# Kernel optimization log

Hardware: AMD Instinct MI355X
Metric: run time of the kernel (lower is better)

The kernel has to match this reference:

```python
import jax, jax.numpy as jnp
import numpy as np

NUM_HEADS = 12


def setup_inputs() -> dict:
    key = jax.random.key(0)
    ks = jax.random.split(key, 6)
    B, N, C = 16, 576, 768
    H, D = NUM_HEADS, 768 // NUM_HEADS
    P = 16
    x = jax.random.normal(ks[0], (B, N, C), dtype=jnp.float32)
    prompt = jax.random.normal(ks[1], (B, 2, P, H, D), dtype=jnp.float32)
    act_scale = jax.random.uniform(ks[2], (2,), dtype=jnp.float32)
    qkv_w = jax.random.normal(ks[3], (3 * C, C), dtype=jnp.float32) * (C ** -0.5)
    proj_w = jax.random.normal(ks[4], (C, C), dtype=jnp.float32) * (C ** -0.5)
    proj_b = jnp.zeros((C,), dtype=jnp.float32)
    return {"x": x, "prompt": prompt, "act_scale": act_scale,
            "qkv_w": qkv_w, "proj_w": proj_w, "proj_b": proj_b}


def reference(x, prompt, act_scale, qkv_w, proj_w, proj_b):
    B, N, C = x.shape
    H = NUM_HEADS
    D = C // H
    scale = D ** -0.5
    # qkv projection: [B,N,3C] -> (3,B,H,N,D)
    qkv = (x @ qkv_w.T).reshape(B, N, 3, H, D).transpose(2, 0, 3, 1, 4)
    q, k, v = qkv[0], qkv[1], qkv[2]
    # prompt: [B,2,P,H,D] -> (2,B,H,P,D)
    pr = jnp.transpose(prompt, (1, 0, 3, 2, 4))
    key_prefix, value_prefix = pr[0], pr[1]        # [B,H,P,D]
    v = jnp.concatenate([value_prefix, v], axis=2)  # [B,H,P+N,D]
    # gated prefix scores
    prompt_attn = jnp.einsum('bhnd,bhpd->bhnp', q, key_prefix) * scale
    prompt_attn = prompt_attn + jnp.tanh(prompt_attn * act_scale[0]) * act_scale[1]
    # standard scores
    attn = jnp.einsum('bhnd,bhmd->bhnm', q, k) * scale
    attn = jnp.concatenate([prompt_attn, attn], axis=-1)  # [B,H,N,P+N]
    attn = jax.nn.softmax(attn, axis=-1)
    out = jnp.einsum('bhnm,bhmd->bhnd', attn, v)  # [B,H,N,D]
    out = out.transpose(0, 2, 1, 3).reshape(B, N, C)
    return out @ proj_w.T + proj_b
```

## Files before the change

### kernel.cpp

```cpp
#include <hip/hip_runtime.h>
#include <hip/hip_bf16.h>
#include <math.h>

namespace {

constexpr int kB = 16, kN = 576, kC = 768, kH = 12, kP = 16;
constexpr int kM = kB * kN;

typedef __attribute__((ext_vector_type(8))) __bf16 bf16x8;
typedef __attribute__((ext_vector_type(4))) float  f32x4;
typedef __attribute__((ext_vector_type(8))) unsigned short u16x8;

__device__ inline unsigned short f2bf(float f) {
  __bf16 h = (__bf16)f;
  return __builtin_bit_cast(unsigned short, h);
}
__device__ inline float bf2f(unsigned short u) {
  unsigned int x = ((unsigned int)u) << 16;
  return __builtin_bit_cast(float, x);
}
__device__ inline unsigned int pk2bf(float lo, float hi) {
  return (unsigned int)f2bf(lo) | ((unsigned int)f2bf(hi) << 16);
}
__device__ inline int xcd_swz(int hw, int nwg) {
  const int per = nwg >> 3;
  return (hw & 7) * per + (hw >> 3);
}

#define GLDS16(src, dst) __builtin_amdgcn_global_load_lds( \
    (const __attribute__((address_space(1))) unsigned int*)(src), \
    (__attribute__((address_space(3))) unsigned int*)(dst), 16, 0, 0)

__global__ __launch_bounds__(256)
void cvt3(const float* __restrict__ x, const float* __restrict__ wq,
          const float* __restrict__ wp, unsigned short* __restrict__ xo,
          unsigned short* __restrict__ wqo, unsigned short* __restrict__ wpo) {
  const int bid = blockIdx.x;
  const float* in; unsigned short* out; int base;
  if (bid < 6912)       { in = x;  out = xo;  base = bid; }
  else if (bid < 8640)  { in = wq; out = wqo; base = bid - 6912; }
  else                  { in = wp; out = wpo; base = bid - 8640; }
  const int i = base * 256 + threadIdx.x;
  const float4 v = ((const float4*)in)[i];
  ((ushort4*)out)[i] = make_ushort4(f2bf(v.x), f2bf(v.y), f2bf(v.z), f2bf(v.w));
}

template<int OB>
__global__ __launch_bounds__(256)
void gemm_bf16(const unsigned short* __restrict__ A, const unsigned short* __restrict__ W,
               const float* __restrict__ bias, void* __restrict__ Yv, int Kd, int Nd) {
  __shared__ __align__(16) unsigned short As[3][4096];
  __shared__ __align__(16) unsigned short Bs[3][4096];
  const int tid  = threadIdx.x;
  const int wv   = tid >> 6, lane = tid & 63;
  const int gx   = Nd >> 7;
  const int lg   = xcd_swz(blockIdx.x, gridDim.x);
  const long bm  = (long)(lg / gx) * 128;
  const long bn  = (long)(lg % gx) * 128;
  const int wr   = (wv >> 1) * 64;
  const int wc   = (wv & 1) * 64;
  const int row15 = lane & 15, kg = lane >> 4;

  auto stage = [&](int buf, int kt) {
#pragma unroll
    for (int site = 0; site < 2; ++site) {
      const int p = site * 256 + tid;
      const unsigned short* srcA = A + (bm + (p >> 2)) * (long)Kd + kt + (p & 3) * 8;
      const unsigned short* srcB = W + (bn + (p >> 2)) * (long)Kd + kt + (p & 3) * 8;
      GLDS16(srcA, &As[buf][site * 2048 + wv * 512]);
      GLDS16(srcB, &Bs[buf][site * 2048 + wv * 512]);
    }
  };

  float bvpre[4] = {0.0f, 0.0f, 0.0f, 0.0f};
  if constexpr (!OB) {
#pragma unroll
    for (int ni = 0; ni < 4; ++ni) bvpre[ni] = bias[bn + wc + ni * 16 + row15];
  }
  asm volatile("s_waitcnt vmcnt(0)" ::: "memory");

  f32x4 acc[4][4] = {};
  stage(0, 0);
  stage(1, 32);

  const int nt = Kd >> 5;
  for (int t = 0; t < nt; ++t) {
    const int cur = t % 3;
    __builtin_amdgcn_sched_barrier(0);
    __builtin_amdgcn_s_barrier();
    if (t + 2 < nt) stage((t + 2) % 3, (t + 2) << 5);
    if (t + 2 < nt)      asm volatile("s_waitcnt vmcnt(8)");
    else if (t + 1 < nt) asm volatile("s_waitcnt vmcnt(4)");
    else                 asm volatile("s_waitcnt vmcnt(0)");
    __builtin_amdgcn_s_barrier();
    __builtin_amdgcn_sched_barrier(0);

    bf16x8 af[4], bf_[4];
#pragma unroll
    for (int mi = 0; mi < 4; ++mi)
      af[mi] = *(const bf16x8*)(&As[cur][(wr + mi * 16 + row15) * 32 + kg * 8]);
#pragma unroll
    for (int ni = 0; ni < 4; ++ni)
      bf_[ni] = *(const bf16x8*)(&Bs[cur][(wc + ni * 16 + row15) * 32 + kg * 8]);
    __builtin_amdgcn_s_setprio(1);
#pragma unroll
    for (int mi = 0; mi < 4; ++mi)
#pragma unroll
      for (int ni = 0; ni < 4; ++ni)
        acc[mi][ni] = __builtin_amdgcn_mfma_f32_16x16x32_bf16(af[mi], bf_[ni], acc[mi][ni], 0, 0, 0);
    __builtin_amdgcn_s_setprio(0);
  }

  const int r4 = kg * 4;
#pragma unroll
  for (int ni = 0; ni < 4; ++ni) {
    const long col = bn + wc + ni * 16 + row15;
    if constexpr (OB) {
      unsigned short* Y = (unsigned short*)Yv;
#pragma unroll
      for (int mi = 0; mi < 4; ++mi)
#pragma unroll
        for (int j = 0; j < 4; ++j)
          Y[(bm + wr + mi * 16 + r4 + j) * (long)Nd + col] = f2bf(acc[mi][ni][j]);
    } else {
      float* Y = (float*)Yv;
#pragma unroll
      for (int mi = 0; mi < 4; ++mi)
#pragma unroll
        for (int j = 0; j < 4; ++j)
          Y[(bm + wr + mi * 16 + r4 + j) * (long)Nd + col] = acc[mi][ni][j] + bvpre[ni];
    }
  }
}

__device__ inline void softmax_group_static(f32x4 (&c)[4], float& lsum,
                                            unsigned short* pl,
                                            const int kg, const int sw) {
  float psum = 0.0f;
#pragma unroll
  for (int kb = 0; kb < 4; ++kb) {
    const float p0 = __expf(c[kb][0] - 10.0f);
    const float p1 = __expf(c[kb][1] - 10.0f);
    const float p2 = __expf(c[kb][2] - 10.0f);
    const float p3 = __expf(c[kb][3] - 10.0f);
    psum += (p0 + p1) + (p2 + p3);
    const int off = (((kb * 2 + (kg >> 1)) ^ sw) << 3) + (kg & 1) * 4;
    *(uint2*)(pl + off) = make_uint2(pk2bf(p0, p1), pk2bf(p2, p3));
  }
  lsum += psum;
}

__global__ __launch_bounds__(192, 3)
void attn_mfma(const unsigned short* __restrict__ qkv, const float* __restrict__ prompt,
               const float* __restrict__ act_scale, unsigned short* __restrict__ attn_out) {
  const int lg = xcd_swz(blockIdx.x, gridDim.x);
  const int qt = lg % 6, bh = lg / 6;
  const int h = bh % kH, b = bh / kH;
  const int tid = threadIdx.x, wv = tid >> 6, lane = tid & 63;
  const int q15 = lane & 15, kg = lane >> 4;

  __shared__ __align__(16) unsigned short Klds[2][4096];
  __shared__ __align__(16) unsigned short Vt[2][4096];
  __shared__ __align__(16) unsigned short Plds[3][2048];

  const float a0 = act_scale[0], a1 = act_scale[1];
  const int sw  = q15 & 7;
  const int sl0 = (kg ^ sw) << 3;
  const int sl1 = ((4 + kg) ^ sw) << 3;

  bf16x8 qf[2][2];
#pragma unroll
  for (int g = 0; g < 2; ++g) {
    const unsigned short* qrow =
        qkv + (size_t)(b * kN + qt * 96 + wv * 32 + g * 16 + q15) * 2304 + h * 64;
#pragma unroll
    for (int dh = 0; dh < 2; ++dh) {
      u16x8 raw = *(const u16x8*)(qrow + dh * 32 + kg * 8);
      u16x8 sc;
#pragma unroll
      for (int j = 0; j < 8; ++j) sc[j] = f2bf(bf2f(raw[j]) * 0.125f);
      qf[g][dh] = __builtin_bit_cast(bf16x8, sc);
    }
  }

  if (tid < 128) {
    const int r = tid >> 3, s = tid & 7;
    const float* src = prompt + (((size_t)(b * 2) * kP + r) * kH + h) * 64 + s * 8;
    const f32x4 f0 = *(const f32x4*)src, f1 = *(const f32x4*)(src + 4);
    *(uint4*)(&Klds[0][r * 64 + ((s ^ (r & 7)) << 3)]) =
        make_uint4(pk2bf(f0[0], f0[1]), pk2bf(f0[2], f0[3]),
                   pk2bf(f1[0], f1[1]), pk2bf(f1[2], f1[3]));
  }
  if (tid < 128) {
    const int kp = tid & 7, vdq = tid >> 3;
    const float* s0 = prompt + (((size_t)(b * 2 + 1) * kP + 2 * kp) * kH + h) * 64 + vdq * 4;
    const f32x4 x0 = *(const f32x4*)s0;
    const f32x4 y0 = *(const f32x4*)(s0 + kH * 64);
#pragma unroll
    for (int j = 0; j < 4; ++j) {
      const int d = vdq * 4 + j;
      *(unsigned int*)(&Vt[0][d * 64 + (((kp >> 2) ^ (d & 7)) << 3) + (kp & 3) * 2]) =
          pk2bf(x0[j], y0[j]);
    }
  }
#pragma unroll
  for (int i = 0; i < 2; ++i) {
    const int idx = tid + 192 * i;
    const int d = idx / 6, szl = (idx % 6) + 2;
    *(uint4*)(&Vt[0][d * 64 + ((szl ^ (d & 7)) << 3)]) = make_uint4(0, 0, 0, 0);
  }
  __syncthreads();

  f32x4 o0[4] = {}, o1[4] = {};
  float l0 = 0.0f, l1 = 0.0f;

  const int vkp  = tid & 31;
  const int vdgb = tid >> 5;
  const int kr8  = lane >> 3, ks8 = lane & 7;

  for (int ch = 0; ch < 10; ++ch) {
    const int cur = ch & 1;

    u16x8 va0, va1, vb0, vb1;
    const bool doV = (ch < 9) && (wv < 2);
    if (ch < 9) {
      if (doV) {
        const unsigned short* r0 = qkv + (size_t)(b * kN + ch * 64 + 2 * vkp) * 2304 + 1536 + h * 64;
        va0 = *(const u16x8*)(r0 + vdgb * 8);
        va1 = *(const u16x8*)(r0 + (vdgb + 4) * 8);
        vb0 = *(const u16x8*)(r0 + 2304 + vdgb * 8);
        vb1 = *(const u16x8*)(r0 + 2304 + (vdgb + 4) * 8);
      } else if (wv == 2) {
#pragma unroll
        for (int g8 = 0; g8 < 8; ++g8) {
          const int r = g8 * 8 + kr8;
          const unsigned short* src =
              qkv + (size_t)(b * kN + ch * 64 + r) * 2304 + 768 + h * 64 + ((ks8 ^ (r & 7)) << 3);
          GLDS16(src, &Klds[cur ^ 1][g8 * 512]);
        }
      }
    }

    f32x4 c0[4], c1[4];
    __builtin_amdgcn_s_setprio(1);
#pragma unroll
    for (int kb = 0; kb < 4; ++kb) {
      if (ch == 0 && kb > 0) {
        c0[kb][0] = c0[kb][1] = c0[kb][2] = c0[kb][3] = -1.0e30f;
        c1[kb][0] = c1[kb][1] = c1[kb][2] = c1[kb][3] = -1.0e30f;
      } else {
        const unsigned short* krow = &Klds[cur][(kb * 16 + q15) * 64];
        const bf16x8 k0 = *(const bf16x8*)(krow + sl0);
        const bf16x8 k1 = *(const bf16x8*)(krow + sl1);
        f32x4 t0 = {}, t1 = {};
        t0 = __builtin_amdgcn_mfma_f32_16x16x32_bf16(k0, qf[0][0], t0, 0, 0, 0);
        c0[kb] = __builtin_amdgcn_mfma_f32_16x16x32_bf16(k1, qf[0][1], t0, 0, 0, 0);
        t1 = __builtin_amdgcn_mfma_f32_16x16x32_bf16(k0, qf[1][0], t1, 0, 0, 0);
        c1[kb] = __builtin_amdgcn_mfma_f32_16x16x32_bf16(k1, qf[1][1], t1, 0, 0, 0);
      }
    }
    __builtin_amdgcn_s_setprio(0);
    if (ch == 0) {
#pragma unroll
      for (int j = 0; j < 4; ++j) {
        const float s0v = c0[0][j];
        const float e0 = __expf(2.0f * s0v * a0);
        c0[0][j] = s0v + ((e0 - 1.0f) / (e0 + 1.0f)) * a1;
        const float s1v = c1[0][j];
        const float e1 = __expf(2.0f * s1v * a0);
        c1[0][j] = s1v + ((e1 - 1.0f) / (e1 + 1.0f)) * a1;
      }
    }

    softmax_group_static(c0, l0, &Plds[wv][q15 * 64], kg, sw);
    softmax_group_static(c1, l1, &Plds[wv][(q15 + 16) * 64], kg, sw);

    if (doV) {
#pragma unroll
      for (int j = 0; j < 8; ++j) {
        const int d0 = vdgb * 8 + j;
        *(unsigned int*)(&Vt[cur ^ 1][d0 * 64 + (((vkp >> 2) ^ (d0 & 7)) << 3) + (vkp & 3) * 2]) =
            (unsigned int)va0[j] | ((unsigned int)vb0[j] << 16);
        const int d1 = (vdgb + 4) * 8 + j;
        *(unsigned int*)(&Vt[cur ^ 1][d1 * 64 + (((vkp >> 2) ^ (d1 & 7)) << 3) + (vkp & 3) * 2]) =
            (unsigned int)va1[j] | ((unsigned int)vb1[j] << 16);
      }
    }

    const unsigned short* p0 = &Plds[wv][q15 * 64];
    const unsigned short* p1 = &Plds[wv][(q15 + 16) * 64];
    const bf16x8 pa00 = *(const bf16x8*)(p0 + sl0);
    const bf16x8 pa01 = *(const bf16x8*)(p0 + sl1);
    const bf16x8 pa10 = *(const bf16x8*)(p1 + sl0);
    const bf16x8 pa11 = *(const bf16x8*)(p1 + sl1);
    __builtin_amdgcn_s_setprio(1);
#pragma unroll
    for (int nb = 0; nb < 4; ++nb) {
      const unsigned short* vr = &Vt[cur][(nb * 16 + q15) * 64];
      const bf16x8 bv0 = *(const bf16x8*)(vr + sl0);
      const bf16x8 bv1 = *(const bf16x8*)(vr + sl1);
      o0[nb] = __builtin_amdgcn_mfma_f32_16x16x32_bf16(pa00, bv0, o0[nb], 0, 0, 0);
      o0[nb] = __builtin_amdgcn_mfma_f32_16x16x32_bf16(pa01, bv1, o0[nb], 0, 0, 0);
      o1[nb] = __builtin_amdgcn_mfma_f32_16x16x32_bf16(pa10, bv0, o1[nb], 0, 0, 0);
      o1[nb] = __builtin_amdgcn_mfma_f32_16x16x32_bf16(pa11, bv1, o1[nb], 0, 0, 0);
    }
    __builtin_amdgcn_s_setprio(0);

    __syncthreads();
  }

  l0 += __shfl_xor(l0, 16, 64);
  l0 += __shfl_xor(l0, 32, 64);
  l1 += __shfl_xor(l1, 16, 64);
  l1 += __shfl_xor(l1, 32, 64);
  const float i0 = 1.0f / l0, i1 = 1.0f / l1;
  float iq0[4], iq1[4];
#pragma unroll
  for (int jr = 0; jr < 4; ++jr) {
    iq0[jr] = __shfl(i0, kg * 4 + jr, 64);
    iq1[jr] = __shfl(i1, kg * 4 + jr, 64);
  }
  unsigned short* ob = attn_out + (size_t)(b * kN + qt * 96 + wv * 32) * 768 + h * 64;
#pragma unroll
  for (int nb = 0; nb < 4; ++nb)
#pragma unroll
    for (int jr = 0; jr < 4; ++jr) {
      ob[(size_t)(kg * 4 + jr) * 768 + nb * 16 + q15] = f2bf(o0[nb][jr] * iq0[jr]);
      ob[(size_t)(16 + kg * 4 + jr) * 768 + nb * 16 + q15] = f2bf(o1[nb][jr] * iq1[jr]);
    }
}

}

extern "C" void kernel_launch(void* const* d_in, const int* in_sizes, int n_in,
                              void* d_out, int out_size, void* d_ws, size_t ws_size,
                              hipStream_t stream) {
  const float* x         = (const float*)d_in[0];
  const float* prompt    = (const float*)d_in[1];
  const float* act_scale = (const float*)d_in[2];
  const float* qkv_w     = (const float*)d_in[3];
  const float* proj_w    = (const float*)d_in[4];
  const float* proj_b    = (const float*)d_in[5];
  float* out = (float*)d_out;

  char* ws = (char*)d_ws;
  unsigned short* qkvb   = (unsigned short*)ws;
  unsigned short* xa     = (unsigned short*)(ws + 42467328);
  unsigned short* qkvwb  = (unsigned short*)(ws + 42467328 + 14155776);
  unsigned short* projwb = (unsigned short*)(ws + 42467328 + 14155776 + 3538944);

  cvt3<<<9216, 256, 0, stream>>>(x, qkv_w, proj_w, xa, qkvwb, projwb);

  gemm_bf16<1><<<(3 * kC / 128) * (kM / 128), 256, 0, stream>>>(xa, qkvwb, nullptr, qkvb, kC, 3 * kC);
  attn_mfma<<<(kN / 96) * kH * kB, 192, 0, stream>>>(qkvb, prompt, act_scale, xa);
  gemm_bf16<0><<<(kC / 128) * (kM / 128), 256, 0, stream>>>(xa, projwb, proj_b, out, kC, kC);
}
```

Measured before the change: 124.3 us.

## Restructure attention into single-wave blocks with register-staged K/V loads

```diff
diff --git a/kernel.cpp b/kernel.cpp
--- a/kernel.cpp
+++ b/kernel.cpp
@@ -150,18 +150,18 @@
   lsum += psum;
 }
 
-__global__ __launch_bounds__(192, 3)
-void attn_mfma(const unsigned short* __restrict__ qkv, const float* __restrict__ prompt,
+__global__ __launch_bounds__(64, 2)
+void attn_wave(const unsigned short* __restrict__ qkv, const float* __restrict__ prompt,
                const float* __restrict__ act_scale, unsigned short* __restrict__ attn_out) {
   const int lg = xcd_swz(blockIdx.x, gridDim.x);
-  const int qt = lg % 6, bh = lg / 6;
+  const int qt = lg % 18, bh = lg / 18;
   const int h = bh % kH, b = bh / kH;
-  const int tid = threadIdx.x, wv = tid >> 6, lane = tid & 63;
+  const int lane = threadIdx.x;
   const int q15 = lane & 15, kg = lane >> 4;
 
-  __shared__ __align__(16) unsigned short Klds[2][4096];
-  __shared__ __align__(16) unsigned short Vt[2][4096];
-  __shared__ __align__(16) unsigned short Plds[3][2048];
+  __shared__ __align__(16) unsigned short Klds[4096];
+  __shared__ __align__(16) unsigned short Vt[4096];
+  __shared__ __align__(16) unsigned short Plds[2048];
 
   const float a0 = act_scale[0], a1 = act_scale[1];
   const int sw  = q15 & 7;
@@ -172,7 +172,7 @@
 #pragma unroll
   for (int g = 0; g < 2; ++g) {
     const unsigned short* qrow =
-        qkv + (size_t)(b * kN + qt * 96 + wv * 32 + g * 16 + q15) * 2304 + h * 64;
+        qkv + (size_t)(b * kN + qt * 32 + g * 16 + q15) * 2304 + h * 64;
 #pragma unroll
     for (int dh = 0; dh < 2; ++dh) {
       u16x8 raw = *(const u16x8*)(qrow + dh * 32 + kg * 8);
@@ -183,80 +183,97 @@
     }
   }
 
-  if (tid < 128) {
-    const int r = tid >> 3, s = tid & 7;
-    const float* src = prompt + (((size_t)(b * 2) * kP + r) * kH + h) * 64 + s * 8;
-    const f32x4 f0 = *(const f32x4*)src, f1 = *(const f32x4*)(src + 4);
-    *(uint4*)(&Klds[0][r * 64 + ((s ^ (r & 7)) << 3)]) =
+  {
+    const int r = lane >> 2, c = lane & 3;
+    const float* src = prompt + (((size_t)(b * 2) * kP + r) * kH + h) * 64 + c * 16;
+    const f32x4 f0 = *(const f32x4*)src,       f1 = *(const f32x4*)(src + 4);
+    const f32x4 f2 = *(const f32x4*)(src + 8), f3 = *(const f32x4*)(src + 12);
+    *(uint4*)&Klds[r * 64 + (((2 * c) ^ (r & 7)) << 3)] =
         make_uint4(pk2bf(f0[0], f0[1]), pk2bf(f0[2], f0[3]),
                    pk2bf(f1[0], f1[1]), pk2bf(f1[2], f1[3]));
-  }
-  if (tid < 128) {
-    const int kp = tid & 7, vdq = tid >> 3;
-    const float* s0 = prompt + (((size_t)(b * 2 + 1) * kP + 2 * kp) * kH + h) * 64 + vdq * 4;
-    const f32x4 x0 = *(const f32x4*)s0;
-    const f32x4 y0 = *(const f32x4*)(s0 + kH * 64);
-#pragma unroll
-    for (int j = 0; j < 4; ++j) {
-      const int d = vdq * 4 + j;
-      *(unsigned int*)(&Vt[0][d * 64 + (((kp >> 2) ^ (d & 7)) << 3) + (kp & 3) * 2]) =
-          pk2bf(x0[j], y0[j]);
-    }
-  }
-#pragma unroll
-  for (int i = 0; i < 2; ++i) {
-    const int idx = tid + 192 * i;
+    *(uint4*)&Klds[r * 64 + (((2 * c + 1) ^ (r & 7)) << 3)] =
+        make_uint4(pk2bf(f2[0], f2[1]), pk2bf(f2[2], f2[3]),
+                   pk2bf(f3[0], f3[1]), pk2bf(f3[2], f3[3]));
+  }
+  {
+    const int kp = lane & 7, vo = lane >> 3;
+    const float* s0 = prompt + (((size_t)(b * 2 + 1) * kP + 2 * kp) * kH + h) * 64 + vo * 8;
+    const float* s1 = s0 + kH * 64;
+    const f32x4 x0 = *(const f32x4*)s0, x1 = *(const f32x4*)(s0 + 4);
+    const f32x4 y0 = *(const f32x4*)s1, y1 = *(const f32x4*)(s1 + 4);
+#pragma unroll
+    for (int e = 0; e < 8; ++e) {
+      const int d = vo * 8 + e;
+      const float xv = (e < 4) ? x0[e & 3] : x1[e & 3];
+      const float yv = (e < 4) ? y0[e & 3] : y1[e & 3];
+      *(unsigned int*)&Vt[d * 64 + (((kp >> 2) ^ (d & 7)) << 3) + (kp & 3) * 2] = pk2bf(xv, yv);
+    }
+  }
+#pragma unroll
+  for (int i = 0; i < 6; ++i) {
+    const int idx = lane * 6 + i;
     const int d = idx / 6, szl = (idx % 6) + 2;
-    *(uint4*)(&Vt[0][d * 64 + ((szl ^ (d & 7)) << 3)]) = make_uint4(0, 0, 0, 0);
-  }
-  __syncthreads();
+    *(uint4*)&Vt[d * 64 + ((szl ^ (d & 7)) << 3)] = make_uint4(0, 0, 0, 0);
+  }
 
   f32x4 o0[4] = {}, o1[4] = {};
   float l0 = 0.0f, l1 = 0.0f;
 
-  const int vkp  = tid & 31;
-  const int vdgb = tid >> 5;
-  const int kr8  = lane >> 3, ks8 = lane & 7;
+  const int vkp = lane & 31, vh = lane >> 5;
+  const int kr8 = lane >> 3, ks8 = lane & 7;
+
+  u16x8 va[4], vb[4];
 
   for (int ch = 0; ch < 10; ++ch) {
-    const int cur = ch & 1;
-
-    u16x8 va0, va1, vb0, vb1;
-    const bool doV = (ch < 9) && (wv < 2);
+    if (ch > 0) {
+      asm volatile("s_waitcnt vmcnt(0)" ::: "memory");
+      __builtin_amdgcn_sched_barrier(0);
+    }
+
+    bf16x8 kf0[4], kf1[4];
+    const int nkb = (ch == 0) ? 1 : 4;
+#pragma unroll
+    for (int kb = 0; kb < 4; ++kb) {
+      if (kb < nkb) {
+        const unsigned short* krow = &Klds[(kb * 16 + q15) * 64];
+        kf0[kb] = *(const bf16x8*)(krow + sl0);
+        kf1[kb] = *(const bf16x8*)(krow + sl1);
+      }
+    }
+    asm volatile("s_waitcnt lgkmcnt(0)" ::: "memory");
+    __builtin_amdgcn_sched_barrier(0);
+
     if (ch < 9) {
-      if (doV) {
-        const unsigned short* r0 = qkv + (size_t)(b * kN + ch * 64 + 2 * vkp) * 2304 + 1536 + h * 64;
-        va0 = *(const u16x8*)(r0 + vdgb * 8);
-        va1 = *(const u16x8*)(r0 + (vdgb + 4) * 8);
-        vb0 = *(const u16x8*)(r0 + 2304 + vdgb * 8);
-        vb1 = *(const u16x8*)(r0 + 2304 + (vdgb + 4) * 8);
-      } else if (wv == 2) {
-#pragma unroll
-        for (int g8 = 0; g8 < 8; ++g8) {
-          const int r = g8 * 8 + kr8;
-          const unsigned short* src =
-              qkv + (size_t)(b * kN + ch * 64 + r) * 2304 + 768 + h * 64 + ((ks8 ^ (r & 7)) << 3);
-          GLDS16(src, &Klds[cur ^ 1][g8 * 512]);
-        }
-      }
+      const unsigned short* r0 =
+          qkv + (size_t)(b * kN + ch * 64 + 2 * vkp) * 2304 + 1536 + h * 64 + vh * 32;
+#pragma unroll
+      for (int j = 0; j < 4; ++j) {
+        va[j] = *(const u16x8*)(r0 + j * 8);
+        vb[j] = *(const u16x8*)(r0 + 2304 + j * 8);
+      }
+#pragma unroll
+      for (int g8 = 0; g8 < 8; ++g8) {
+        const int r = g8 * 8 + kr8;
+        const unsigned short* src =
+            qkv + (size_t)(b * kN + ch * 64 + r) * 2304 + 768 + h * 64 + ((ks8 ^ (r & 7)) << 3);
+        GLDS16(src, &Klds[g8 * 512]);
+      }
+      __builtin_amdgcn_sched_barrier(0);
     }
 
     f32x4 c0[4], c1[4];
     __builtin_amdgcn_s_setprio(1);
 #pragma unroll
     for (int kb = 0; kb < 4; ++kb) {
-      if (ch == 0 && kb > 0) {
+      if (kb < nkb) {
+        f32x4 t0 = {}, t1 = {};
+        t0 = __builtin_amdgcn_mfma_f32_16x16x32_bf16(kf0[kb], qf[0][0], t0, 0, 0, 0);
+        c0[kb] = __builtin_amdgcn_mfma_f32_16x16x32_bf16(kf1[kb], qf[0][1], t0, 0, 0, 0);
+        t1 = __builtin_amdgcn_mfma_f32_16x16x32_bf16(kf0[kb], qf[1][0], t1, 0, 0, 0);
+        c1[kb] = __builtin_amdgcn_mfma_f32_16x16x32_bf16(kf1[kb], qf[1][1], t1, 0, 0, 0);
+      } else {
         c0[kb][0] = c0[kb][1] = c0[kb][2] = c0[kb][3] = -1.0e30f;
         c1[kb][0] = c1[kb][1] = c1[kb][2] = c1[kb][3] = -1.0e30f;
-      } else {
-        const unsigned short* krow = &Klds[cur][(kb * 16 + q15) * 64];
-        const bf16x8 k0 = *(const bf16x8*)(krow + sl0);
-        const bf16x8 k1 = *(const bf16x8*)(krow + sl1);
-        f32x4 t0 = {}, t1 = {};
-        t0 = __builtin_amdgcn_mfma_f32_16x16x32_bf16(k0, qf[0][0], t0, 0, 0, 0);
-        c0[kb] = __builtin_amdgcn_mfma_f32_16x16x32_bf16(k1, qf[0][1], t0, 0, 0, 0);
-        t1 = __builtin_amdgcn_mfma_f32_16x16x32_bf16(k0, qf[1][0], t1, 0, 0, 0);
-        c1[kb] = __builtin_amdgcn_mfma_f32_16x16x32_bf16(k1, qf[1][1], t1, 0, 0, 0);
       }
     }
     __builtin_amdgcn_s_setprio(0);
@@ -272,41 +289,46 @@
       }
     }
 
-    softmax_group_static(c0, l0, &Plds[wv][q15 * 64], kg, sw);
-    softmax_group_static(c1, l1, &Plds[wv][(q15 + 16) * 64], kg, sw);
-
-    if (doV) {
-#pragma unroll
-      for (int j = 0; j < 8; ++j) {
-        const int d0 = vdgb * 8 + j;
-        *(unsigned int*)(&Vt[cur ^ 1][d0 * 64 + (((vkp >> 2) ^ (d0 & 7)) << 3) + (vkp & 3) * 2]) =
-            (unsigned int)va0[j] | ((unsigned int)vb0[j] << 16);
-        const int d1 = (vdgb + 4) * 8 + j;
-        *(unsigned int*)(&Vt[cur ^ 1][d1 * 64 + (((vkp >> 2) ^ (d1 & 7)) << 3) + (vkp & 3) * 2]) =
-            (unsigned int)va1[j] | ((unsigned int)vb1[j] << 16);
-      }
-    }
-
-    const unsigned short* p0 = &Plds[wv][q15 * 64];
-    const unsigned short* p1 = &Plds[wv][(q15 + 16) * 64];
+    softmax_group_static(c0, l0, &Plds[q15 * 64], kg, sw);
+    softmax_group_static(c1, l1, &Plds[(q15 + 16) * 64], kg, sw);
+
+    const unsigned short* p0 = &Plds[q15 * 64];
+    const unsigned short* p1 = &Plds[(q15 + 16) * 64];
     const bf16x8 pa00 = *(const bf16x8*)(p0 + sl0);
     const bf16x8 pa01 = *(const bf16x8*)(p0 + sl1);
     const bf16x8 pa10 = *(const bf16x8*)(p1 + sl0);
     const bf16x8 pa11 = *(const bf16x8*)(p1 + sl1);
+    bf16x8 bv0[4], bv1[4];
+#pragma unroll
+    for (int nb = 0; nb < 4; ++nb) {
+      const unsigned short* vr = &Vt[(nb * 16 + q15) * 64];
+      bv0[nb] = *(const bf16x8*)(vr + sl0);
+      bv1[nb] = *(const bf16x8*)(vr + sl1);
+    }
+    asm volatile("s_waitcnt lgkmcnt(0)" ::: "memory");
+    __builtin_amdgcn_sched_barrier(0);
     __builtin_amdgcn_s_setprio(1);
 #pragma unroll
     for (int nb = 0; nb < 4; ++nb) {
-      const unsigned short* vr = &Vt[cur][(nb * 16 + q15) * 64];
-      const bf16x8 bv0 = *(const bf16x8*)(vr + sl0);
-      const bf16x8 bv1 = *(const bf16x8*)(vr + sl1);
-      o0[nb] = __builtin_amdgcn_mfma_f32_16x16x32_bf16(pa00, bv0, o0[nb], 0, 0, 0);
-      o0[nb] = __builtin_amdgcn_mfma_f32_16x16x32_bf16(pa01, bv1, o0[nb], 0, 0, 0);
-      o1[nb] = __builtin_amdgcn_mfma_f32_16x16x32_bf16(pa10, bv0, o1[nb], 0, 0, 0);
-      o1[nb] = __builtin_amdgcn_mfma_f32_16x16x32_bf16(pa11, bv1, o1[nb], 0, 0, 0);
+      o0[nb] = __builtin_amdgcn_mfma_f32_16x16x32_bf16(pa00, bv0[nb], o0[nb], 0, 0, 0);
+      o0[nb] = __builtin_amdgcn_mfma_f32_16x16x32_bf16(pa01, bv1[nb], o0[nb], 0, 0, 0);
+      o1[nb] = __builtin_amdgcn_mfma_f32_16x16x32_bf16(pa10, bv0[nb], o1[nb], 0, 0, 0);
+      o1[nb] = __builtin_amdgcn_mfma_f32_16x16x32_bf16(pa11, bv1[nb], o1[nb], 0, 0, 0);
     }
     __builtin_amdgcn_s_setprio(0);
 
-    __syncthreads();
+    if (ch < 9) {
+      asm volatile("s_waitcnt vmcnt(8)" ::: "memory");
+      __builtin_amdgcn_sched_barrier(0);
+#pragma unroll
+      for (int j = 0; j < 4; ++j)
+#pragma unroll
+        for (int e = 0; e < 8; ++e) {
+          const int d = vh * 32 + j * 8 + e;
+          *(unsigned int*)&Vt[d * 64 + (((vkp >> 2) ^ (d & 7)) << 3) + (vkp & 3) * 2] =
+              (unsigned int)va[j][e] | ((unsigned int)vb[j][e] << 16);
+        }
+    }
   }
 
   l0 += __shfl_xor(l0, 16, 64);
@@ -320,7 +342,7 @@
     iq0[jr] = __shfl(i0, kg * 4 + jr, 64);
     iq1[jr] = __shfl(i1, kg * 4 + jr, 64);
   }
-  unsigned short* ob = attn_out + (size_t)(b * kN + qt * 96 + wv * 32) * 768 + h * 64;
+  unsigned short* ob = attn_out + (size_t)(b * kN + qt * 32) * 768 + h * 64;
 #pragma unroll
   for (int nb = 0; nb < 4; ++nb)
 #pragma unroll
@@ -352,6 +374,6 @@
   cvt3<<<9216, 256, 0, stream>>>(x, qkv_w, proj_w, xa, qkvwb, projwb);
 
   gemm_bf16<1><<<(3 * kC / 128) * (kM / 128), 256, 0, stream>>>(xa, qkvwb, nullptr, qkvb, kC, 3 * kC);
-  attn_mfma<<<(kN / 96) * kH * kB, 192, 0, stream>>>(qkvb, prompt, act_scale, xa);
+  attn_wave<<<(kN / 32) * kH * kB, 64, 0, stream>>>(qkvb, prompt, act_scale, xa);
   gemm_bf16<0><<<(kC / 128) * (kM / 128), 256, 0, stream>>>(xa, projwb, proj_b, out, kC, kC);
 }
```

Result: slower. 138.0 us (+11.0%).

## Double attention query tile to 192 rows with six waves per block

Applied to the files above, without the earlier changes.

```diff
diff --git a/kernel.cpp b/kernel.cpp
--- a/kernel.cpp
+++ b/kernel.cpp
@@ -150,18 +150,18 @@
   lsum += psum;
 }
 
-__global__ __launch_bounds__(192, 3)
+__global__ __launch_bounds__(384)
 void attn_mfma(const unsigned short* __restrict__ qkv, const float* __restrict__ prompt,
                const float* __restrict__ act_scale, unsigned short* __restrict__ attn_out) {
   const int lg = xcd_swz(blockIdx.x, gridDim.x);
-  const int qt = lg % 6, bh = lg / 6;
+  const int qt = lg % 3, bh = lg / 3;
   const int h = bh % kH, b = bh / kH;
   const int tid = threadIdx.x, wv = tid >> 6, lane = tid & 63;
   const int q15 = lane & 15, kg = lane >> 4;
 
   __shared__ __align__(16) unsigned short Klds[2][4096];
   __shared__ __align__(16) unsigned short Vt[2][4096];
-  __shared__ __align__(16) unsigned short Plds[3][2048];
+  __shared__ __align__(16) unsigned short Plds[6][2048];
 
   const float a0 = act_scale[0], a1 = act_scale[1];
   const int sw  = q15 & 7;
@@ -172,7 +172,7 @@
 #pragma unroll
   for (int g = 0; g < 2; ++g) {
     const unsigned short* qrow =
-        qkv + (size_t)(b * kN + qt * 96 + wv * 32 + g * 16 + q15) * 2304 + h * 64;
+        qkv + (size_t)(b * kN + qt * 192 + wv * 32 + g * 16 + q15) * 2304 + h * 64;
 #pragma unroll
     for (int dh = 0; dh < 2; ++dh) {
       u16x8 raw = *(const u16x8*)(qrow + dh * 32 + kg * 8);
@@ -203,10 +203,8 @@
           pk2bf(x0[j], y0[j]);
     }
   }
-#pragma unroll
-  for (int i = 0; i < 2; ++i) {
-    const int idx = tid + 192 * i;
-    const int d = idx / 6, szl = (idx % 6) + 2;
+  {
+    const int d = tid / 6, szl = (tid % 6) + 2;
     *(uint4*)(&Vt[0][d * 64 + ((szl ^ (d & 7)) << 3)]) = make_uint4(0, 0, 0, 0);
   }
   __syncthreads();
@@ -214,29 +212,29 @@
   f32x4 o0[4] = {}, o1[4] = {};
   float l0 = 0.0f, l1 = 0.0f;
 
-  const int vkp  = tid & 31;
-  const int vdgb = tid >> 5;
-  const int kr8  = lane >> 3, ks8 = lane & 7;
+  const int vkp = (wv & 3) * 8 + (lane >> 3);
+  const int vdg = lane & 7;
+  const int kr8 = lane >> 3, ks8 = lane & 7;
 
   for (int ch = 0; ch < 10; ++ch) {
     const int cur = ch & 1;
 
-    u16x8 va0, va1, vb0, vb1;
-    const bool doV = (ch < 9) && (wv < 2);
+    u16x8 va, vb;
+    const bool doV = (ch < 9) && (wv < 4);
     if (ch < 9) {
       if (doV) {
-        const unsigned short* r0 = qkv + (size_t)(b * kN + ch * 64 + 2 * vkp) * 2304 + 1536 + h * 64;
-        va0 = *(const u16x8*)(r0 + vdgb * 8);
-        va1 = *(const u16x8*)(r0 + (vdgb + 4) * 8);
-        vb0 = *(const u16x8*)(r0 + 2304 + vdgb * 8);
-        vb1 = *(const u16x8*)(r0 + 2304 + (vdgb + 4) * 8);
-      } else if (wv == 2) {
-#pragma unroll
-        for (int g8 = 0; g8 < 8; ++g8) {
-          const int r = g8 * 8 + kr8;
+        const unsigned short* r0 =
+            qkv + (size_t)(b * kN + ch * 64 + 2 * vkp) * 2304 + 1536 + h * 64 + vdg * 8;
+        va = *(const u16x8*)r0;
+        vb = *(const u16x8*)(r0 + 2304);
+      } else if (wv >= 4) {
+        const int rbase = (wv - 4) * 32;
+#pragma unroll
+        for (int g4 = 0; g4 < 4; ++g4) {
+          const int r = rbase + g4 * 8 + kr8;
           const unsigned short* src =
               qkv + (size_t)(b * kN + ch * 64 + r) * 2304 + 768 + h * 64 + ((ks8 ^ (r & 7)) << 3);
-          GLDS16(src, &Klds[cur ^ 1][g8 * 512]);
+          GLDS16(src, &Klds[cur ^ 1][(rbase + g4 * 8) * 64]);
         }
       }
     }
@@ -278,12 +276,9 @@
     if (doV) {
 #pragma unroll
       for (int j = 0; j < 8; ++j) {
-        const int d0 = vdgb * 8 + j;
-        *(unsigned int*)(&Vt[cur ^ 1][d0 * 64 + (((vkp >> 2) ^ (d0 & 7)) << 3) + (vkp & 3) * 2]) =
-            (unsigned int)va0[j] | ((unsigned int)vb0[j] << 16);
-        const int d1 = (vdgb + 4) * 8 + j;
-        *(unsigned int*)(&Vt[cur ^ 1][d1 * 64 + (((vkp >> 2) ^ (d1 & 7)) << 3) + (vkp & 3) * 2]) =
-            (unsigned int)va1[j] | ((unsigned int)vb1[j] << 16);
+        const int d = vdg * 8 + j;
+        *(unsigned int*)(&Vt[cur ^ 1][d * 64 + (((vkp >> 2) ^ (d & 7)) << 3) + (vkp & 3) * 2]) =
+            (unsigned int)va[j] | ((unsigned int)vb[j] << 16);
       }
     }
 
@@ -320,7 +315,7 @@
     iq0[jr] = __shfl(i0, kg * 4 + jr, 64);
     iq1[jr] = __shfl(i1, kg * 4 + jr, 64);
   }
-  unsigned short* ob = attn_out + (size_t)(b * kN + qt * 96 + wv * 32) * 768 + h * 64;
+  unsigned short* ob = attn_out + (size_t)(b * kN + qt * 192 + wv * 32) * 768 + h * 64;
 #pragma unroll
   for (int nb = 0; nb < 4; ++nb)
 #pragma unroll
@@ -352,6 +347,6 @@
   cvt3<<<9216, 256, 0, stream>>>(x, qkv_w, proj_w, xa, qkvwb, projwb);
 
   gemm_bf16<1><<<(3 * kC / 128) * (kM / 128), 256, 0, stream>>>(xa, qkvwb, nullptr, qkvb, kC, 3 * kC);
-  attn_mfma<<<(kN / 96) * kH * kB, 192, 0, stream>>>(qkvb, prompt, act_scale, xa);
+  attn_mfma<<<(kN / 192) * kH * kB, 384, 0, stream>>>(qkvb, prompt, act_scale, xa);
   gemm_bf16<0><<<(kC / 128) * (kM / 128), 256, 0, stream>>>(xa, projwb, proj_b, out, kC, kC);
 }
```

Result: slower. 140.7 us (+13.2%).

## Use BK=64 double-buffered GEMM tiles with XOR-swizzled LDS layout

Applied to the files above, without the earlier changes.

```diff
diff --git a/kernel.cpp b/kernel.cpp
--- a/kernel.cpp
+++ b/kernel.cpp
@@ -49,8 +49,8 @@
 __global__ __launch_bounds__(256)
 void gemm_bf16(const unsigned short* __restrict__ A, const unsigned short* __restrict__ W,
                const float* __restrict__ bias, void* __restrict__ Yv, int Kd, int Nd) {
-  __shared__ __align__(16) unsigned short As[3][4096];
-  __shared__ __align__(16) unsigned short Bs[3][4096];
+  __shared__ __align__(16) unsigned short As[2][8192];
+  __shared__ __align__(16) unsigned short Bs[2][8192];
   const int tid  = threadIdx.x;
   const int wv   = tid >> 6, lane = tid & 63;
   const int gx   = Nd >> 7;
@@ -63,12 +63,12 @@
 
   auto stage = [&](int buf, int kt) {
 #pragma unroll
-    for (int site = 0; site < 2; ++site) {
-      const int p = site * 256 + tid;
-      const unsigned short* srcA = A + (bm + (p >> 2)) * (long)Kd + kt + (p & 3) * 8;
-      const unsigned short* srcB = W + (bn + (p >> 2)) * (long)Kd + kt + (p & 3) * 8;
-      GLDS16(srcA, &As[buf][site * 2048 + wv * 512]);
-      GLDS16(srcB, &Bs[buf][site * 2048 + wv * 512]);
+    for (int site = 0; site < 4; ++site) {
+      const int u = site * 256 + tid;
+      const int row = u >> 3, slot = u & 7;
+      const int ksw = kt + (((slot ^ (row & 7)) << 3));
+      GLDS16(A + (bm + row) * (long)Kd + ksw, &As[buf][site * 2048 + wv * 512]);
+      GLDS16(W + (bn + row) * (long)Kd + ksw, &Bs[buf][site * 2048 + wv * 512]);
     }
   };
 
@@ -81,33 +81,41 @@
 
   f32x4 acc[4][4] = {};
   stage(0, 0);
-  stage(1, 32);
-
-  const int nt = Kd >> 5;
+
+  const int sw8 = row15 & 7;
+  const int nt = Kd >> 6;
   for (int t = 0; t < nt; ++t) {
-    const int cur = t % 3;
+    const int cur = t & 1;
     __builtin_amdgcn_sched_barrier(0);
     __builtin_amdgcn_s_barrier();
-    if (t + 2 < nt) stage((t + 2) % 3, (t + 2) << 5);
-    if (t + 2 < nt)      asm volatile("s_waitcnt vmcnt(8)");
-    else if (t + 1 < nt) asm volatile("s_waitcnt vmcnt(4)");
+    if (t + 1 < nt) stage(cur ^ 1, (t + 1) << 6);
+    if (t + 1 < nt)      asm volatile("s_waitcnt vmcnt(8)");
     else                 asm volatile("s_waitcnt vmcnt(0)");
     __builtin_amdgcn_s_barrier();
     __builtin_amdgcn_sched_barrier(0);
 
-    bf16x8 af[4], bf_[4];
+    bf16x8 af[4][2], bf_[4][2];
 #pragma unroll
     for (int mi = 0; mi < 4; ++mi)
-      af[mi] = *(const bf16x8*)(&As[cur][(wr + mi * 16 + row15) * 32 + kg * 8]);
+#pragma unroll
+      for (int ks = 0; ks < 2; ++ks)
+        af[mi][ks] = *(const bf16x8*)(&As[cur][(wr + mi * 16 + row15) * 64 +
+                                               (((ks * 4 + kg) ^ sw8) << 3)]);
 #pragma unroll
     for (int ni = 0; ni < 4; ++ni)
-      bf_[ni] = *(const bf16x8*)(&Bs[cur][(wc + ni * 16 + row15) * 32 + kg * 8]);
+#pragma unroll
+      for (int ks = 0; ks < 2; ++ks)
+        bf_[ni][ks] = *(const bf16x8*)(&Bs[cur][(wc + ni * 16 + row15) * 64 +
+                                                (((ks * 4 + kg) ^ sw8) << 3)]);
     __builtin_amdgcn_s_setprio(1);
 #pragma unroll
-    for (int mi = 0; mi < 4; ++mi)
-#pragma unroll
-      for (int ni = 0; ni < 4; ++ni)
-        acc[mi][ni] = __builtin_amdgcn_mfma_f32_16x16x32_bf16(af[mi], bf_[ni], acc[mi][ni], 0, 0, 0);
+    for (int ks = 0; ks < 2; ++ks)
+#pragma unroll
+      for (int mi = 0; mi < 4; ++mi)
+#pragma unroll
+        for (int ni = 0; ni < 4; ++ni)
+          acc[mi][ni] = __builtin_amdgcn_mfma_f32_16x16x32_bf16(af[mi][ks], bf_[ni][ks],
+                                                                acc[mi][ni], 0, 0, 0);
     __builtin_amdgcn_s_setprio(0);
   }
 
```

New measurement: 119.5 us. 1.04x faster.
